# Performance work log

Measured on AMD Instinct MI355X. Metric: run time of the kernel, lower is better.

## Reference

```python
import jax, jax.numpy as jnp
import numpy as np

BN_EPS = 1e-5


def _get_normals(radius, nsample, xyz):
    # xyz: [B, N, 3] -> normals [B, N, 3] (eigenvector of smallest eigenvalue)
    B, N, _ = xyz.shape
    sq = jnp.sum(xyz * xyz, axis=-1)                      # [B, N]
    sqrdists = sq[:, :, None] + sq[:, None, :] - 2.0 * jnp.einsum('bnc,bmc->bnm', xyz, xyz)
    ar = jnp.arange(N, dtype=jnp.int32)
    group_idx = jnp.where(sqrdists > radius * radius, N, ar[None, None, :])  # [B, N, N]
    group_idx = jnp.sort(group_idx, axis=-1)[:, :, :nsample]                 # [B, N, ns]
    group_idx = jnp.where(group_idx == N, group_idx[:, :, :1], group_idx)
    group_points = jax.vmap(lambda pts, idx: pts[idx])(xyz, group_idx)       # [B, N, ns, 3]
    centered = group_points - group_points.mean(axis=2, keepdims=True)
    cov = jnp.einsum('bnsc,bnsd->bncd', centered, centered)                  # [B, N, 3, 3]
    _, eigen_vectors = jnp.linalg.eigh(cov)
    return eigen_vectors[..., 0]


def _conv_bn(h, w, b, g, be, m, v, relu=True):
    # h: [B, N, Cin]; 1x1 Conv1d == per-point linear; BN in eval mode
    h = h @ w.T + b
    h = (h - m) / jnp.sqrt(v + BN_EPS) * g + be
    return jax.nn.relu(h) if relu else h


def setup_inputs() -> dict:
    key = jax.random.key(0)
    ks = jax.random.split(key, 32)
    B, N = 4, 4096
    inp = {
        'x': jax.random.uniform(ks[0], (B, N, 3), dtype=jnp.float32),
        'small': 0.2,
        'large': 0.3,
    }
    chans = [(1, 16), (16, 32), (32, 16), (16, 1)]
    for li, (cin, cout) in enumerate(chans, start=1):
        k = 4 * li
        inp[f'w{li}'] = jax.random.normal(ks[k], (cout, cin), dtype=jnp.float32) * (1.0 / np.sqrt(cin))
        inp[f'b{li}'] = jax.random.normal(ks[k + 1], (cout,), dtype=jnp.float32) * 0.1
        inp[f'g{li}'] = jax.random.uniform(ks[k + 2], (cout,), dtype=jnp.float32) + 0.5
        inp[f'be{li}'] = jax.random.normal(ks[k + 3], (cout,), dtype=jnp.float32) * 0.1
        inp[f'm{li}'] = jnp.zeros((cout,), dtype=jnp.float32)
        inp[f'v{li}'] = jnp.ones((cout,), dtype=jnp.float32)
    return inp


def reference(x, small, large,
              w1, b1, g1, be1, m1, v1,
              w2, b2, g2, be2, m2, v2,
              w3, b3, g3, be3, m3, v3,
              w4, b4, g4, be4, m4, v4):
    xyz = x[:, :, :3]
    small_n = _get_normals(small, 32, xyz)   # [B, N, 3]
    large_n = _get_normals(large, 64, xyz)
    curvature = jnp.linalg.norm((small_n - large_n) * 0.5, axis=2)  # [B, N]
    h = curvature[..., None]                                        # [B, N, 1]
    h = _conv_bn(h, w1, b1, g1, be1, m1, v1)
    h = _conv_bn(h, w2, b2, g2, be2, m2, v2)
    h = _conv_bn(h, w3, b3, g3, be3, m3, v3)
    h = _conv_bn(h, w4, b4, g4, be4, m4, v4, relu=False)
    return h[..., 0]                                                # [B, N]
```

## Files before the change

### kernel.cpp

```cpp
#include <hip/hip_runtime.h>
#include <math.h>

#define BLAS_FMA 1
#define SYR2_VARIANT 0

#define DEV static __device__ __forceinline__

DEV float fA(float a, float b){ return __fadd_rn(a,b); }
DEV float fSb(float a, float b){ return __fsub_rn(a,b); }
DEV float fM(float a, float b){ return __fmul_rn(a,b); }
DEV float fDv(float a, float b){ return __fdiv_rn(a,b); }
DEV float fQ(float a){ return __fsqrt_rn(a); }
DEV float fF(float a, float b, float c){ return __builtin_fmaf(a,b,c); }
DEV float fSGN(float a, float b){ return copysignf(a,b); }

DEV float slapy2f(float x, float y){
  float xa=fabsf(x), ya=fabsf(y);
  float w=fmaxf(xa,ya), z=fminf(xa,ya);
  if (z==0.0f) return w;
  float t=fDv(z,w);
  return fM(w, fQ(fA(1.0f, fM(t,t))));
}

DEV void slartgf(float f, float g, float* c, float* s, float* r){
  const float safmin=1.17549435e-38f;
  const float safmax=8.50705917e+37f;
  const float rtmin=1.08420217e-19f;
  const float rtmax=6.52169543e+18f;
  float f1=fabsf(f), g1=fabsf(g);
  if (g==0.0f){ *c=1.0f; *s=0.0f; *r=f; }
  else if (f==0.0f){ *c=0.0f; *s=fSGN(1.0f,g); *r=g1; }
  else {
    if (f1>rtmin && f1<rtmax && g1>rtmin && g1<rtmax){
      float d=fQ(fA(fM(f,f), fM(g,g)));
      *c=fDv(f1,d);
      *r=fSGN(d,f);
      *s=fDv(g,*r);
    } else {
      float u=fminf(safmax, fmaxf(safmin, fmaxf(f1,g1)));
      float fs=fDv(f,u), gs=fDv(g,u);
      float d=fQ(fA(fM(fs,fs), fM(gs,gs)));
      *c=fDv(fabsf(fs), d);
      *r=fSGN(d,f);
      *s=fDv(gs,*r);
      *r=fM(*r,u);
    }
  }
}

DEV void slaev2f(float a, float b, float c, float* rt1, float* rt2, float* cs1, float* sn1){
  float sm=fA(a,c);
  float df=fSb(a,c);
  float adf=fabsf(df);
  float tb=fA(b,b);
  float ab=fabsf(tb);
  float acmx, acmn;
  if (fabsf(a)>fabsf(c)){ acmx=a; acmn=c; } else { acmx=c; acmn=a; }
  float rt;
  if (adf>ab){ float t=fDv(ab,adf); rt=fM(adf, fQ(fA(1.0f, fM(t,t)))); }
  else if (adf<ab){ float t=fDv(adf,ab); rt=fM(ab, fQ(fA(1.0f, fM(t,t)))); }
  else { rt=fM(ab, fQ(2.0f)); }
  int sgn1;
  if (sm<0.0f){
    *rt1=fM(0.5f, fSb(sm,rt)); sgn1=-1;
    *rt2=fSb(fM(fDv(acmx,*rt1),acmn), fM(fDv(b,*rt1),b));
  } else if (sm>0.0f){
    *rt1=fM(0.5f, fA(sm,rt)); sgn1=1;
    *rt2=fSb(fM(fDv(acmx,*rt1),acmn), fM(fDv(b,*rt1),b));
  } else {
    *rt1=fM(0.5f,rt); *rt2=fM(-0.5f,rt); sgn1=1;
  }
  float cs; int sgn2;
  if (df>=0.0f){ cs=fA(df,rt); sgn2=1; } else { cs=fSb(df,rt); sgn2=-1; }
  float acs=fabsf(cs);
  if (acs>ab){
    float ct=fDv(-tb,cs);
    *sn1=fDv(1.0f, fQ(fA(1.0f, fM(ct,ct))));
    *cs1=fM(ct,*sn1);
  } else {
    if (ab==0.0f){ *cs1=1.0f; *sn1=0.0f; }
    else {
      float tn=fDv(-cs,tb);
      *cs1=fDv(1.0f, fQ(fA(1.0f, fM(tn,tn))));
      *sn1=fM(tn,*cs1);
    }
  }
  if (sgn1==sgn2){ float tn=*cs1; *cs1=-(*sn1); *sn1=tn; }
}

DEV void eig3_smallest(float a00, float a10, float a20, float a11, float a21, float a22,
                       float* vout){
  const float RMIN=3.13916472e-16f;
  const float RMAX=3.18559313e+15f;
  float anrm=fmaxf(fabsf(a00), fmaxf(fabsf(a10), fmaxf(fabsf(a20),
             fmaxf(fabsf(a11), fmaxf(fabsf(a21), fabsf(a22))))));
  if (anrm>0.0f && anrm<RMIN){
    float sig=fDv(RMIN,anrm);
    a00=fM(a00,sig); a10=fM(a10,sig); a20=fM(a20,sig);
    a11=fM(a11,sig); a21=fM(a21,sig); a22=fM(a22,sig);
  } else if (anrm>RMAX){
    float sig=fDv(RMAX,anrm);
    a00=fM(a00,sig); a10=fM(a10,sig); a20=fM(a20,sig);
    a11=fM(a11,sig); a21=fM(a21,sig); a22=fM(a22,sig);
  }
  float d0,d1,d2, e0,e1;
  float tau1=0.0f, hv2=0.0f;
  {
    float xnorm=fabsf(a20);
    if (xnorm==0.0f){
      tau1=0.0f;
      d0=a00; d1=a11; d2=a22;
      e0=a10; e1=a21;
    } else {
      float alpha=a10;
      float beta=-fSGN(slapy2f(alpha,xnorm), alpha);
      tau1=fDv(fSb(beta,alpha), beta);
      float rs=fDv(1.0f, fSb(alpha,beta));
      hv2=fM(a20, rs);
      float t2a=fM(a21, hv2);
#if BLAS_FMA
      float w1=fF(tau1, t2a, fM(tau1, a11));
      float w2=fF(fM(tau1,hv2), a22, fM(tau1, a21));
      float sd=fF(hv2, w2, w1);
#else
      float w1=fA(fM(tau1,a11), fM(tau1,t2a));
      float w2=fA(fM(tau1,a21), fM(fM(tau1,hv2),a22));
      float sd=fA(w1, fM(w2,hv2));
#endif
      float al2=fM(fM(-0.5f,tau1), sd);
      float nw1=fA(w1, al2);
#if BLAS_FMA
      float nw2=fF(al2, hv2, w2);
#else
      float nw2=fA(w2, fM(al2,hv2));
#endif
      w1=nw1; w2=nw2;
      float b11, b21, b22;
#if SYR2_VARIANT==0
      b11=fA(a11, fM(-2.0f, w1));
      b21=fA(a21, fF(hv2, -w1, -w2));
      b22=fA(a22, fF(hv2, -w2, fM(w2, -hv2)));
#elif SYR2_VARIANT==1
      b11=fSb(fSb(a11, w1), w1);
      b21=fSb(fF(hv2, -w1, a21), w2);
      b22=fF(w2, -hv2, fF(hv2, -w2, a22));
#else
      b11=fA(fA(a11, -w1), -w1);
      b21=fA(fA(a21, fM(hv2,-w1)), -w2);
      b22=fA(fA(a22, fM(hv2,-w2)), fM(w2,-hv2));
#endif
      d0=a00; d1=b11; d2=b22;
      e0=beta; e1=b21;
    }
  }
  float z0=1.0f,z1=0.0f,z2=0.0f, z3=0.0f,z4=1.0f,z5=0.0f, z6=0.0f,z7=0.0f,z8=1.0f;

#define DGET(iA)   ((iA)==0?d0:((iA)==1?d1:d2))
#define DSET(iA,vA) do{ float _dsv=(vA); int _dsi=(iA); \
  d0=(_dsi==0)?_dsv:d0; d1=(_dsi==1)?_dsv:d1; d2=(_dsi==2)?_dsv:d2; }while(0)
#define EGET(iA)   ((iA)==0?e0:e1)
#define ESET(iA,vA) do{ float _esv=(vA); int _esi=(iA); \
  e0=(_esi==0)?_esv:e0; e1=(_esi==1)?_esv:e1; }while(0)
#define ZGET(rA,cA) ((cA)==0? ((rA)==0?z0:((rA)==1?z1:z2)) : ((cA)==1? ((rA)==0?z3:((rA)==1?z4:z5)) : ((rA)==0?z6:((rA)==1?z7:z8))))
#define ZSET(rA,cA,vA) do{ float _zsv=(vA); int _zsr=(rA), _zsc=(cA); \
  z0=(_zsr==0&&_zsc==0)?_zsv:z0; z1=(_zsr==1&&_zsc==0)?_zsv:z1; z2=(_zsr==2&&_zsc==0)?_zsv:z2; \
  z3=(_zsr==0&&_zsc==1)?_zsv:z3; z4=(_zsr==1&&_zsc==1)?_zsv:z4; z5=(_zsr==2&&_zsc==1)?_zsv:z5; \
  z6=(_zsr==0&&_zsc==2)?_zsv:z6; z7=(_zsr==1&&_zsc==2)?_zsv:z7; z8=(_zsr==2&&_zsc==2)?_zsv:z8; }while(0)
#define ZROT0(ccA,ssA) do{ float _zc=(ccA), _zs=(ssA); \
  float _t0=z3, _a0=z0; z3=fSb(fM(_zc,_t0),fM(_zs,_a0)); z0=fA(fM(_zs,_t0),fM(_zc,_a0)); \
  float _t1=z4, _a1=z1; z4=fSb(fM(_zc,_t1),fM(_zs,_a1)); z1=fA(fM(_zs,_t1),fM(_zc,_a1)); \
  float _t2=z5, _a2=z2; z5=fSb(fM(_zc,_t2),fM(_zs,_a2)); z2=fA(fM(_zs,_t2),fM(_zc,_a2)); }while(0)
#define ZROT1(ccA,ssA) do{ float _zc=(ccA), _zs=(ssA); \
  float _t0=z6, _a0=z3; z6=fSb(fM(_zc,_t0),fM(_zs,_a0)); z3=fA(fM(_zs,_t0),fM(_zc,_a0)); \
  float _t1=z7, _a1=z4; z7=fSb(fM(_zc,_t1),fM(_zs,_a1)); z4=fA(fM(_zs,_t1),fM(_zc,_a1)); \
  float _t2=z8, _a2=z5; z8=fSb(fM(_zc,_t2),fM(_zs,_a2)); z5=fA(fM(_zs,_t2),fM(_zc,_a2)); }while(0)
#define ZSWAPC(caA,cbA) do{ int _zwa=(caA), _zwb=(cbA); \
  _Pragma("unroll") \
  for (int _zwr=0;_zwr<3;++_zwr){ \
    float _zwta=ZGET(_zwr,_zwa); float _zwtb=ZGET(_zwr,_zwb); \
    ZSET(_zwr,_zwa,_zwtb); ZSET(_zwr,_zwb,_zwta); \
  } }while(0)

  const float EPS=5.96046448e-08f;
  const float EPS2=3.55271368e-15f;
  const float SAFMIN=1.17549435e-38f;
  const float SSFMAX=3.07445735e+18f;
  const float SSFMIN=3.05175781e-05f;
  int l1=1, jtot=0; const int nmaxit=90;
  bool skip_sort=false;
  while (l1<=3){
    if (l1>1) ESET(l1-2, 0.0f);
    int m=3;
    for (int mm=l1; mm<=2; ++mm){
      float tst=fabsf(EGET(mm-1));
      if (tst==0.0f){ m=mm; break; }
      if (tst<=fM(fM(fQ(fabsf(DGET(mm-1))), fQ(fabsf(DGET(mm)))), EPS)){ ESET(mm-1,0.0f); m=mm; break; }
    }
    int l=l1, lsv=l, lend=m, lendsv=m;
    l1=m+1;
    if (lend==l) continue;
    float anorm=fabsf(DGET(lend-1));
    for (int i=l; i<=lend-1; ++i){ anorm=fmaxf(anorm,fabsf(DGET(i-1))); anorm=fmaxf(anorm,fabsf(EGET(i-1))); }
    if (anorm==0.0f) continue;
    int iscale=0;
    if (anorm>SSFMAX){
      iscale=1; float mv=fDv(SSFMAX,anorm);
      for (int i=l;i<=lend;++i) DSET(i-1, fM(DGET(i-1),mv));
      for (int i=l;i<=lend-1;++i) ESET(i-1, fM(EGET(i-1),mv));
    } else if (anorm<SSFMIN){
      iscale=2; float mv=fDv(SSFMIN,anorm);
      for (int i=l;i<=lend;++i) DSET(i-1, fM(DGET(i-1),mv));
      for (int i=l;i<=lend-1;++i) ESET(i-1, fM(EGET(i-1),mv));
    }
    if (fabsf(DGET(lend-1))<fabsf(DGET(l-1))){ lend=lsv; l=lendsv; }
    if (lend>l){
      for (;;){
        int M=lend;
        if (l!=lend){
          for (int mm=l; mm<=lend-1; ++mm){
            float ee=fabsf(EGET(mm-1));
            float tst=fM(ee,ee);
            if (tst<=fA(fM(fM(EPS2,fabsf(DGET(mm-1))), fabsf(DGET(mm))), SAFMIN)){ M=mm; break; }
          }
        }
        if (M<lend) ESET(M-1,0.0f);
        float p=DGET(l-1);
        if (M==l){
          l+=1;
          if (l<=lend) continue; else break;
        }
        if (M==l+1){
          float rt1,rt2,cc,ss;
          if (l==1){
            slaev2f(d0, e0, d1, &rt1,&rt2,&cc,&ss);
            ZROT0(cc, ss);
            d0=rt1; d1=rt2; e0=0.0f;
          } else {
            slaev2f(d1, e1, d2, &rt1,&rt2,&cc,&ss);
            ZROT1(cc, ss);
            d1=rt1; d2=rt2; e1=0.0f;
          }
          l+=2;
          if (l<=lend) continue; else break;
        }
        if (jtot==nmaxit) break;
        ++jtot;
        float g=fDv(fSb(d1,p), fM(2.0f,e0));
        float r=slapy2f(g,1.0f);
        g=fA(fSb(d2,p), fDv(e0, fA(g, fSGN(r,g))));
        float s=1.0f, c=1.0f; p=0.0f;
        float cr0,cr1,sr0,sr1;
        {
          float f=fM(s,e1);
          float bb=fM(c,e1);
          slartgf(g,f,&c,&s,&r);
          g=fSb(d2,p);
          r=fA(fM(fSb(d1,g),s), fM(fM(2.0f,c),bb));
          p=fM(s,r);
          d2=fA(g,p);
          g=fSb(fM(c,r),bb);
          cr1=c; sr1=-s;
        }
        {
          float f=fM(s,e0);
          float bb=fM(c,e0);
          slartgf(g,f,&c,&s,&r);
          e1=r;
          g=fSb(d1,p);
          r=fA(fM(fSb(d0,g),s), fM(fM(2.0f,c),bb));
          p=fM(s,r);
          d1=fA(g,p);
          g=fSb(fM(c,r),bb);
          cr0=c; sr0=-s;
        }
        if (cr1!=1.0f || sr1!=0.0f) ZROT1(cr1, sr1);
        if (cr0!=1.0f || sr0!=0.0f) ZROT0(cr0, sr0);
        d0=fSb(d0,p);
        e0=g;
      }
    } else {
      for (;;){
        int M=lend;
        if (l!=lend){
          for (int mm=l; mm>=lend+1; --mm){
            float ee=fabsf(EGET(mm-2));
            float tst=fM(ee,ee);
            if (tst<=fA(fM(fM(EPS2,fabsf(DGET(mm-1))), fabsf(DGET(mm-2))), SAFMIN)){ M=mm; break; }
          }
        }
        if (M>lend) ESET(M-2,0.0f);
        float p=DGET(l-1);
        if (M==l){
          l-=1;
          if (l>=lend) continue; else break;
        }
        if (M==l-1){
          float rt1,rt2,cc,ss;
          if (l==3){
            slaev2f(d1, e1, d2, &rt1,&rt2,&cc,&ss);
            ZROT1(cc, ss);
            d1=rt1; d2=rt2; e1=0.0f;
          } else {
            slaev2f(d0, e0, d1, &rt1,&rt2,&cc,&ss);
            ZROT0(cc, ss);
            d0=rt1; d1=rt2; e0=0.0f;
          }
          l-=2;
          if (l>=lend) continue; else break;
        }
        if (jtot==nmaxit) break;
        ++jtot;
        float g=fDv(fSb(d1,p), fM(2.0f,e1));
        float r=slapy2f(g,1.0f);
        g=fA(fSb(d0,p), fDv(e1, fA(g, fSGN(r,g))));
        float s=1.0f, c=1.0f; p=0.0f;
        float cr0,cr1,sr0,sr1;
        {
          float f=fM(s,e0);
          float bb=fM(c,e0);
          slartgf(g,f,&c,&s,&r);
          g=fSb(d0,p);
          r=fA(fM(fSb(d1,g),s), fM(fM(2.0f,c),bb));
          p=fM(s,r);
          d0=fA(g,p);
          g=fSb(fM(c,r),bb);
          cr0=c; sr0=s;
        }
        {
          float f=fM(s,e1);
          float bb=fM(c,e1);
          slartgf(g,f,&c,&s,&r);
          e0=r;
          g=fSb(d1,p);
          r=fA(fM(fSb(d2,g),s), fM(fM(2.0f,c),bb));
          p=fM(s,r);
          d1=fA(g,p);
          g=fSb(fM(c,r),bb);
          cr1=c; sr1=s;
        }
        if (cr0!=1.0f || sr0!=0.0f) ZROT0(cr0, sr0);
        if (cr1!=1.0f || sr1!=0.0f) ZROT1(cr1, sr1);
        d2=fSb(d2,p);
        e1=g;
      }
    }
    if (iscale==1){
      float mv=fDv(anorm,SSFMAX);
      for (int i=lsv;i<=lendsv;++i) DSET(i-1, fM(DGET(i-1),mv));
      for (int i=lsv;i<=lendsv-1;++i) ESET(i-1, fM(EGET(i-1),mv));
    } else if (iscale==2){
      float mv=fDv(anorm,SSFMIN);
      for (int i=lsv;i<=lendsv;++i) DSET(i-1, fM(DGET(i-1),mv));
      for (int i=lsv;i<=lendsv-1;++i) ESET(i-1, fM(EGET(i-1),mv));
    }
    if (jtot>=nmaxit){ skip_sort=true; break; }
  }
  if (!skip_sort){
    for (int ii=2; ii<=3; ++ii){
      int i=ii-1, k=i; float p=DGET(i-1);
      for (int j=ii; j<=3; ++j) if (DGET(j-1)<p){ k=j; p=DGET(j-1); }
      if (k!=i){
        DSET(k-1, DGET(i-1)); DSET(i-1, p);
        ZSWAPC(i-1, k-1);
      }
    }
  }
  float o0=z0, o1=z1, o2=z2;
  if (tau1!=0.0f){
#if BLAS_FMA
    float wv=fF(hv2, o2, o1);
    float t2=fM(-tau1, wv);
    o1=fA(o1, t2);
    o2=fF(t2, hv2, o2);
#else
    float wv=fA(o1, fM(o2,hv2));
    float t2=fM(-tau1, wv);
    o1=fA(o1, t2);
    o2=fA(o2, fM(hv2,t2));
#endif
  }
  vout[0]=o0; vout[1]=o1; vout[2]=o2;
#undef DGET
#undef DSET
#undef EGET
#undef ESET
#undef ZGET
#undef ZSET
#undef ZROT0
#undef ZROT1
#undef ZSWAPC
}

struct KP {
  const float* x; const float* rs; const float* rl;
  const float *w1,*b1,*g1,*be1,*m1,*v1;
  const float *w2,*b2,*g2,*be2,*m2,*v2;
  const float *w3,*b3,*g3,*be3,*m3,*v3;
  const float *w4,*b4,*g4,*be4,*m4,*v4;
  float* out;
};

#define WS_STRIDE 128

__global__ __launch_bounds__(64) void scan_kernel(const float* __restrict__ x,
                                                  const float* __restrict__ rsp,
                                                  const float* __restrict__ rlp,
                                                  unsigned short* __restrict__ ws){
  const int lane=threadIdx.x;
  const int pt=blockIdx.x;
  const int b=pt>>12, n=pt&4095;
  const float* P=x+(size_t)b*(4096*3);
  const double rds=rint((double)rsp[0]*1e7)/1e7;
  const double rdl=rint((double)rlp[0]*1e7)/1e7;
  const float rr_s=(float)(rds*rds);
  const float rr_l=(float)(rdl*rdl);
  const float px=P[3*n], py=P[3*n+1], pz=P[3*n+2];
  const float sqn=fA(fA(fM(px,px),fM(py,py)),fM(pz,pz));
  unsigned short* w=ws+(size_t)pt*WS_STRIDE;
  int cs=0, cl=0;
  for (int c=0;c<64;++c){
    int j=c*64+lane;
    float qx=P[3*j], qy=P[3*j+1], qz=P[3*j+2];
    float sqj=fA(fA(fM(qx,qx),fM(qy,qy)),fM(qz,qz));
    float dot=fA(fA(fM(px,qx),fM(py,qy)),fM(pz,qz));
    float d2=fSb(fA(sqn,sqj), fM(2.0f,dot));
    bool pl=!(d2>rr_l);
    bool ps=!(d2>rr_s);
    unsigned long long bl=__ballot(pl);
    unsigned long long bs=__ballot(ps);
    unsigned long long ltm=(1ull<<lane)-1ull;
    int posl=cl+__popcll(bl&ltm);
    int poss=cs+__popcll(bs&ltm);
    if (pl&&posl<64) w[posl]=(unsigned short)j;
    if (ps&&poss<32) w[64+poss]=(unsigned short)j;
    cl+=__popcll(bl); if(cl>64) cl=64;
    cs+=__popcll(bs); if(cs>32) cs=32;
    if (cs>=32&&cl>=64) break;
  }
  if (lane==0){ w[96]=(unsigned short)cl; w[97]=(unsigned short)cs; }
}

__global__ __launch_bounds__(64) void momeig_kernel(KP kp,
                                                    const unsigned short* __restrict__ ws){
  const int lane=threadIdx.x;
  const int t=blockIdx.x*64+lane;
  const int p=t>>1, which=t&1;
  const int b=p>>12;
  const float* P=kp.x+(size_t)b*(4096*3);
  const unsigned char* recB=(const unsigned char*)(ws+(size_t)p*WS_STRIDE);
  const uint4* q=(const uint4*)(recB + (which? 0 : 128));
  uint4 v0=q[0], v1=q[1], v2=q[2], v3=q[3];
  uint4 v4=q[4], v5=q[5], v6=q[6], v7=q[7];
  const unsigned int cw=*(const unsigned int*)(recB+192);
  const int cnt = which? (int)(cw&0xFFFFu) : (int)(cw>>16);
  const int trip= which? 64 : 32;
  unsigned int a[32]={v0.x,v0.y,v0.z,v0.w, v1.x,v1.y,v1.z,v1.w,
                      v2.x,v2.y,v2.z,v2.w, v3.x,v3.y,v3.z,v3.w,
                      v4.x,v4.y,v4.z,v4.w, v5.x,v5.y,v5.z,v5.w,
                      v6.x,v6.y,v6.z,v6.w, v7.x,v7.y,v7.z,v7.w};
  const int j0=(int)(a[0]&0xFFFFu);

  float sx=0.0f, sy=0.0f, sz=0.0f;
#pragma unroll
  for (int k=0;k<64;++k){
    int raw=(k&1)? (int)(a[k>>1]>>16) : (int)(a[k>>1]&0xFFFFu);
    int idx=(k<cnt)? raw : j0;
    float cx=P[3*idx], cy=P[3*idx+1], cz=P[3*idx+2];
    float nx=fA(sx,cx), ny=fA(sy,cy), nz=fA(sz,cz);
    bool en=(k<trip);
    sx=en?nx:sx; sy=en?ny:sy; sz=en?nz:sz;
  }
  const float dv=which? 64.0f : 32.0f;
  const float mx=fDv(sx,dv), my=fDv(sy,dv), mz=fDv(sz,dv);

  float c0=0,c1=0,c2=0,c3=0,c4=0,c5=0;
#pragma unroll
  for (int k=0;k<64;++k){
    int raw=(k&1)? (int)(a[k>>1]>>16) : (int)(a[k>>1]&0xFFFFu);
    int idx=(k<cnt)? raw : j0;
    float cx=fSb(P[3*idx],mx), cy=fSb(P[3*idx+1],my), cz=fSb(P[3*idx+2],mz);
    float t0=fA(c0,fM(cx,cx)), t1=fA(c1,fM(cy,cx)), t2=fA(c2,fM(cz,cx));
    float t3=fA(c3,fM(cy,cy)), t4=fA(c4,fM(cz,cy)), t5=fA(c5,fM(cz,cz));
    bool en=(k<trip);
    c0=en?t0:c0; c1=en?t1:c1; c2=en?t2:c2;
    c3=en?t3:c3; c4=en?t4:c4; c5=en?t5:c5;
  }

  float v[3];
  eig3_smallest(c0,c1,c2,c3,c4,c5,v);

  float pn0=__shfl_xor(v[0],1);
  float pn1=__shfl_xor(v[1],1);
  float pn2=__shfl_xor(v[2],1);

  if ((lane&1)==0){
    float dx=fM(fSb(v[0],pn0),0.5f);
    float dy=fM(fSb(v[1],pn1),0.5f);
    float dz=fM(fSb(v[2],pn2),0.5f);
    float curv=fQ(fA(fA(fM(dx,dx),fM(dy,dy)),fM(dz,dz)));

    float h1[16];
#pragma unroll
    for (int j=0;j<16;++j){
      float a0=fA(fM(kp.w1[j],curv), kp.b1[j]);
      a0=fA(fM(fDv(fSb(a0,kp.m1[j]), fQ(fA(kp.v1[j],1e-5f))), kp.g1[j]), kp.be1[j]);
      h1[j]=fmaxf(a0,0.0f);
    }
    float h2[32];
#pragma unroll
    for (int j=0;j<32;++j){
      float a0=0.0f;
#pragma unroll
      for (int k=0;k<16;++k) a0=fF(h1[k], kp.w2[j*16+k], a0);
      a0=fA(a0, kp.b2[j]);
      a0=fA(fM(fDv(fSb(a0,kp.m2[j]), fQ(fA(kp.v2[j],1e-5f))), kp.g2[j]), kp.be2[j]);
      h2[j]=fmaxf(a0,0.0f);
    }
    float h3[16];
#pragma unroll
    for (int j=0;j<16;++j){
      float a0=0.0f;
#pragma unroll
      for (int k=0;k<32;++k) a0=fF(h2[k], kp.w3[j*32+k], a0);
      a0=fA(a0, kp.b3[j]);
      a0=fA(fM(fDv(fSb(a0,kp.m3[j]), fQ(fA(kp.v3[j],1e-5f))), kp.g3[j]), kp.be3[j]);
      h3[j]=fmaxf(a0,0.0f);
    }
    float o=0.0f;
#pragma unroll
    for (int k=0;k<16;++k) o=fF(h3[k], kp.w4[k], o);
    o=fA(o, kp.b4[0]);
    o=fA(fM(fDv(fSb(o,kp.m4[0]), fQ(fA(kp.v4[0],1e-5f))), kp.g4[0]), kp.be4[0]);
    kp.out[p]=o;
  }
}

__global__ __launch_bounds__(256) void freq_kernel(KP kp){
  __shared__ float sP[4096*3];
  __shared__ float sSq[4096];
  __shared__ unsigned short sIdxL[64][66];
  __shared__ unsigned short sIdxS[64][34];
  __shared__ unsigned char sCntL[64], sCntS[64];
  const int tid=threadIdx.x;
  const int lane=tid&63, wid=tid>>6;
  const int b=blockIdx.x>>6;
  const int n0=(blockIdx.x&63)*64;
  const float* P=kp.x+(size_t)b*(4096*3);
  for (int i=tid;i<4096*3;i+=256) sP[i]=P[i];
  for (int j=tid;j<4096;j+=256){
    float qx=P[3*j],qy=P[3*j+1],qz=P[3*j+2];
    sSq[j]=fA(fA(fM(qx,qx),fM(qy,qy)),fM(qz,qz));
  }
  __syncthreads();
  const double rds=rint((double)kp.rs[0]*1e7)/1e7;
  const double rdl=rint((double)kp.rl[0]*1e7)/1e7;
  const float rr_s=(float)(rds*rds);
  const float rr_l=(float)(rdl*rdl);
  for (int pi=0; pi<16; ++pi){
    const int pl_i=wid*16+pi;
    const int n=n0+pl_i;
    const float px=sP[3*n], py=sP[3*n+1], pz=sP[3*n+2];
    const float sqn=sSq[n];
    int cs=0, cl=0;
    for (int c=0;c<64;++c){
      int j=c*64+lane;
      float dot=fA(fA(fM(px,sP[3*j]),fM(py,sP[3*j+1])),fM(pz,sP[3*j+2]));
      float d2=fSb(fA(sqn,sSq[j]), fM(2.0f,dot));
      bool pl_=!(d2>rr_l);
      bool ps_=!(d2>rr_s);
      unsigned long long bl=__ballot(pl_);
      unsigned long long bs=__ballot(ps_);
      unsigned long long ltm=(1ull<<lane)-1ull;
      int posl=cl+__popcll(bl&ltm);
      int poss=cs+__popcll(bs&ltm);
      if (pl_&&posl<64) sIdxL[pl_i][posl]=(unsigned short)j;
      if (ps_&&poss<32) sIdxS[pl_i][poss]=(unsigned short)j;
      cl+=__popcll(bl); if(cl>64) cl=64;
      cs+=__popcll(bs); if(cs>32) cs=32;
      if (cs>=32&&cl>=64) break;
    }
    if (lane==0){ sCntL[pl_i]=(unsigned char)cl; sCntS[pl_i]=(unsigned char)cs; }
  }
  __syncthreads();
  if (lane<16){
    const int pl_i=wid*16+lane;
    const int ptg=blockIdx.x*64+pl_i;
    const int csn=sCntS[pl_i], cln=sCntL[pl_i];
    const int j0s=sIdxS[pl_i][0], j0l=sIdxL[pl_i][0];
    float ssx=0.0f,ssy=0.0f,ssz=0.0f, slx=0.0f,sly=0.0f,slz=0.0f;
    for (int k=0;k<32;++k){
      int idx=(k<csn)?(int)sIdxS[pl_i][k]:j0s;
      ssx=fA(ssx,sP[3*idx]); ssy=fA(ssy,sP[3*idx+1]); ssz=fA(ssz,sP[3*idx+2]);
    }
    for (int k=0;k<64;++k){
      int idx=(k<cln)?(int)sIdxL[pl_i][k]:j0l;
      slx=fA(slx,sP[3*idx]); sly=fA(sly,sP[3*idx+1]); slz=fA(slz,sP[3*idx+2]);
    }
    const float msx=fDv(ssx,32.0f), msy=fDv(ssy,32.0f), msz=fDv(ssz,32.0f);
    const float mlx=fDv(slx,64.0f), mly=fDv(sly,64.0f), mlz=fDv(slz,64.0f);
    float sc0=0,sc1=0,sc2=0,sc3=0,sc4=0,sc5=0;
    for (int k=0;k<32;++k){
      int idx=(k<csn)?(int)sIdxS[pl_i][k]:j0s;
      float cx=fSb(sP[3*idx],msx), cy=fSb(sP[3*idx+1],msy), cz=fSb(sP[3*idx+2],msz);
      sc0=fA(sc0,fM(cx,cx)); sc1=fA(sc1,fM(cy,cx)); sc2=fA(sc2,fM(cz,cx));
      sc3=fA(sc3,fM(cy,cy)); sc4=fA(sc4,fM(cz,cy)); sc5=fA(sc5,fM(cz,cz));
    }
    float lc0=0,lc1=0,lc2=0,lc3=0,lc4=0,lc5=0;
    for (int k=0;k<64;++k){
      int idx=(k<cln)?(int)sIdxL[pl_i][k]:j0l;
      float cx=fSb(sP[3*idx],mlx), cy=fSb(sP[3*idx+1],mly), cz=fSb(sP[3*idx+2],mlz);
      lc0=fA(lc0,fM(cx,cx)); lc1=fA(lc1,fM(cy,cx)); lc2=fA(lc2,fM(cz,cx));
      lc3=fA(lc3,fM(cy,cy)); lc4=fA(lc4,fM(cz,cy)); lc5=fA(lc5,fM(cz,cz));
    }
    float snv[3], lnv[3];
    eig3_smallest(sc0,sc1,sc2,sc3,sc4,sc5, snv);
    eig3_smallest(lc0,lc1,lc2,lc3,lc4,lc5, lnv);
    float dx=fM(fSb(snv[0],lnv[0]),0.5f);
    float dy=fM(fSb(snv[1],lnv[1]),0.5f);
    float dz=fM(fSb(snv[2],lnv[2]),0.5f);
    float curv=fQ(fA(fA(fM(dx,dx),fM(dy,dy)),fM(dz,dz)));
    float h1[16];
#pragma unroll
    for (int j=0;j<16;++j){
      float a0=fA(fM(kp.w1[j],curv), kp.b1[j]);
      a0=fA(fM(fDv(fSb(a0,kp.m1[j]), fQ(fA(kp.v1[j],1e-5f))), kp.g1[j]), kp.be1[j]);
      h1[j]=fmaxf(a0,0.0f);
    }
    float h2[32];
#pragma unroll
    for (int j=0;j<32;++j){
      float a0=0.0f;
#pragma unroll
      for (int k=0;k<16;++k) a0=fF(h1[k], kp.w2[j*16+k], a0);
      a0=fA(a0, kp.b2[j]);
      a0=fA(fM(fDv(fSb(a0,kp.m2[j]), fQ(fA(kp.v2[j],1e-5f))), kp.g2[j]), kp.be2[j]);
      h2[j]=fmaxf(a0,0.0f);
    }
    float h3[16];
#pragma unroll
    for (int j=0;j<16;++j){
      float a0=0.0f;
#pragma unroll
      for (int k=0;k<32;++k) a0=fF(h2[k], kp.w3[j*32+k], a0);
      a0=fA(a0, kp.b3[j]);
      a0=fA(fM(fDv(fSb(a0,kp.m3[j]), fQ(fA(kp.v3[j],1e-5f))), kp.g3[j]), kp.be3[j]);
      h3[j]=fmaxf(a0,0.0f);
    }
    float o=0.0f;
#pragma unroll
    for (int k=0;k<16;++k) o=fF(h3[k], kp.w4[k], o);
    o=fA(o, kp.b4[0]);
    o=fA(fM(fDv(fSb(o,kp.m4[0]), fQ(fA(kp.v4[0],1e-5f))), kp.g4[0]), kp.be4[0]);
    kp.out[ptg]=o;
  }
}

extern "C" void kernel_launch(void* const* d_in, const int* in_sizes, int n_in,
                              void* d_out, int out_size, void* d_ws, size_t ws_size,
                              hipStream_t stream){
  (void)n_in; (void)out_size;
  KP kp;
  kp.x  =(const float*)d_in[0];
  kp.rs =(const float*)d_in[1];
  kp.rl =(const float*)d_in[2];
  kp.w1 =(const float*)d_in[3];  kp.b1 =(const float*)d_in[4];  kp.g1 =(const float*)d_in[5];
  kp.be1=(const float*)d_in[6];  kp.m1 =(const float*)d_in[7];  kp.v1 =(const float*)d_in[8];
  kp.w2 =(const float*)d_in[9];  kp.b2 =(const float*)d_in[10]; kp.g2 =(const float*)d_in[11];
  kp.be2=(const float*)d_in[12]; kp.m2 =(const float*)d_in[13]; kp.v2 =(const float*)d_in[14];
  kp.w3 =(const float*)d_in[15]; kp.b3 =(const float*)d_in[16]; kp.g3 =(const float*)d_in[17];
  kp.be3=(const float*)d_in[18]; kp.m3 =(const float*)d_in[19]; kp.v3 =(const float*)d_in[20];
  kp.w4 =(const float*)d_in[21]; kp.b4 =(const float*)d_in[22]; kp.g4 =(const float*)d_in[23];
  kp.be4=(const float*)d_in[24]; kp.m4 =(const float*)d_in[25]; kp.v4 =(const float*)d_in[26];
  kp.out=(float*)d_out;
  const int BN=in_sizes[0]/3;
  const size_t ws_need=(size_t)BN*256;
  if (ws_size>=ws_need){
    unsigned short* wsA=(unsigned short*)d_ws;
    scan_kernel<<<BN, 64, 0, stream>>>(kp.x, kp.rs, kp.rl, wsA);
    momeig_kernel<<<BN/32, 64, 0, stream>>>(kp, wsA);
  } else {
    freq_kernel<<<BN/64, 256, 0, stream>>>(kp);
  }
}
```

Baseline: 179.2 us.

## Add SoA preprocessing pass and store neighbor coordinates instead of indices

Adds a pre-pass that turns the xyz points into structure-of-arrays form with precomputed squared norms, so the scan kernel reads points with coalesced loads and no longer recomputes the norms. The scan kernel now writes neighbor coordinates straight into a larger per-point record instead of 16-bit indices, so the moment/eigen kernel reads its neighbors contiguously rather than gathering them by index. In exchange the workspace grows about fourfold, there is one extra kernel launch, and the scan kernel issues more global writes.

```diff
diff --git a/kernel.cpp b/kernel.cpp
--- a/kernel.cpp
+++ b/kernel.cpp
@@ -400,28 +400,43 @@
   float* out;
 };
 
-#define WS_STRIDE 128
-
-__global__ __launch_bounds__(64) void scan_kernel(const float* __restrict__ x,
-                                                  const float* __restrict__ rsp,
+#define REC_F 296
+
+__global__ __launch_bounds__(256) void soa_kernel(const float* __restrict__ x,
+                                                  float* __restrict__ xs, float* __restrict__ ys,
+                                                  float* __restrict__ zs, float* __restrict__ sq,
+                                                  int BN){
+  int i=blockIdx.x*256+threadIdx.x;
+  if (i<BN){
+    float a=x[3*i], b=x[3*i+1], c=x[3*i+2];
+    xs[i]=a; ys[i]=b; zs[i]=c;
+    sq[i]=fA(fA(fM(a,a),fM(b,b)),fM(c,c));
+  }
+}
+
+__global__ __launch_bounds__(64) void scan_kernel(const float* __restrict__ rsp,
                                                   const float* __restrict__ rlp,
-                                                  unsigned short* __restrict__ ws){
+                                                  float* __restrict__ wsA,
+                                                  const float* __restrict__ xs,
+                                                  const float* __restrict__ ys,
+                                                  const float* __restrict__ zs,
+                                                  const float* __restrict__ sq){
   const int lane=threadIdx.x;
   const int pt=blockIdx.x;
   const int b=pt>>12, n=pt&4095;
-  const float* P=x+(size_t)b*(4096*3);
+  const int g0=b<<12;
   const double rds=rint((double)rsp[0]*1e7)/1e7;
   const double rdl=rint((double)rlp[0]*1e7)/1e7;
   const float rr_s=(float)(rds*rds);
   const float rr_l=(float)(rdl*rdl);
-  const float px=P[3*n], py=P[3*n+1], pz=P[3*n+2];
-  const float sqn=fA(fA(fM(px,px),fM(py,py)),fM(pz,pz));
-  unsigned short* w=ws+(size_t)pt*WS_STRIDE;
+  const float px=xs[g0+n], py=ys[g0+n], pz=zs[g0+n];
+  const float sqn=sq[g0+n];
+  float* w=wsA+(size_t)pt*REC_F;
   int cs=0, cl=0;
   for (int c=0;c<64;++c){
-    int j=c*64+lane;
-    float qx=P[3*j], qy=P[3*j+1], qz=P[3*j+2];
-    float sqj=fA(fA(fM(qx,qx),fM(qy,qy)),fM(qz,qz));
+    int gj=g0+c*64+lane;
+    float qx=xs[gj], qy=ys[gj], qz=zs[gj];
+    float sqj=sq[gj];
     float dot=fA(fA(fM(px,qx),fM(py,qy)),fM(pz,qz));
     float d2=fSb(fA(sqn,sqj), fM(2.0f,dot));
     bool pl=!(d2>rr_l);
@@ -431,41 +446,31 @@
     unsigned long long ltm=(1ull<<lane)-1ull;
     int posl=cl+__popcll(bl&ltm);
     int poss=cs+__popcll(bs&ltm);
-    if (pl&&posl<64) w[posl]=(unsigned short)j;
-    if (ps&&poss<32) w[64+poss]=(unsigned short)j;
+    if (pl&&posl<64){ w[posl*3]=qx; w[posl*3+1]=qy; w[posl*3+2]=qz; }
+    if (ps&&poss<32){ w[192+poss*3]=qx; w[192+poss*3+1]=qy; w[192+poss*3+2]=qz; }
     cl+=__popcll(bl); if(cl>64) cl=64;
     cs+=__popcll(bs); if(cs>32) cs=32;
     if (cs>=32&&cl>=64) break;
   }
-  if (lane==0){ w[96]=(unsigned short)cl; w[97]=(unsigned short)cs; }
+  if (lane==0){ ((unsigned*)w)[288]=(unsigned)cl | ((unsigned)cs<<16); }
 }
 
 __global__ __launch_bounds__(64) void momeig_kernel(KP kp,
-                                                    const unsigned short* __restrict__ ws){
+                                                    const float* __restrict__ wsA){
   const int lane=threadIdx.x;
   const int t=blockIdx.x*64+lane;
   const int p=t>>1, which=t&1;
-  const int b=p>>12;
-  const float* P=kp.x+(size_t)b*(4096*3);
-  const unsigned char* recB=(const unsigned char*)(ws+(size_t)p*WS_STRIDE);
-  const uint4* q=(const uint4*)(recB + (which? 0 : 128));
-  uint4 v0=q[0], v1=q[1], v2=q[2], v3=q[3];
-  uint4 v4=q[4], v5=q[5], v6=q[6], v7=q[7];
-  const unsigned int cw=*(const unsigned int*)(recB+192);
+  const float* rec=wsA+(size_t)p*REC_F;
+  const unsigned cw=((const unsigned*)rec)[288];
   const int cnt = which? (int)(cw&0xFFFFu) : (int)(cw>>16);
   const int trip= which? 64 : 32;
-  unsigned int a[32]={v0.x,v0.y,v0.z,v0.w, v1.x,v1.y,v1.z,v1.w,
-                      v2.x,v2.y,v2.z,v2.w, v3.x,v3.y,v3.z,v3.w,
-                      v4.x,v4.y,v4.z,v4.w, v5.x,v5.y,v5.z,v5.w,
-                      v6.x,v6.y,v6.z,v6.w, v7.x,v7.y,v7.z,v7.w};
-  const int j0=(int)(a[0]&0xFFFFu);
+  const float* cf = rec + (which? 0 : 192);
 
   float sx=0.0f, sy=0.0f, sz=0.0f;
 #pragma unroll
   for (int k=0;k<64;++k){
-    int raw=(k&1)? (int)(a[k>>1]>>16) : (int)(a[k>>1]&0xFFFFu);
-    int idx=(k<cnt)? raw : j0;
-    float cx=P[3*idx], cy=P[3*idx+1], cz=P[3*idx+2];
+    int kk=(k<cnt)? k : 0;
+    float cx=cf[3*kk], cy=cf[3*kk+1], cz=cf[3*kk+2];
     float nx=fA(sx,cx), ny=fA(sy,cy), nz=fA(sz,cz);
     bool en=(k<trip);
     sx=en?nx:sx; sy=en?ny:sy; sz=en?nz:sz;
@@ -476,9 +481,8 @@
   float c0=0,c1=0,c2=0,c3=0,c4=0,c5=0;
 #pragma unroll
   for (int k=0;k<64;++k){
-    int raw=(k&1)? (int)(a[k>>1]>>16) : (int)(a[k>>1]&0xFFFFu);
-    int idx=(k<cnt)? raw : j0;
-    float cx=fSb(P[3*idx],mx), cy=fSb(P[3*idx+1],my), cz=fSb(P[3*idx+2],mz);
+    int kk=(k<cnt)? k : 0;
+    float cx=fSb(cf[3*kk],mx), cy=fSb(cf[3*kk+1],my), cz=fSb(cf[3*kk+2],mz);
     float t0=fA(c0,fM(cx,cx)), t1=fA(c1,fM(cy,cx)), t2=fA(c2,fM(cz,cx));
     float t3=fA(c3,fM(cy,cy)), t4=fA(c4,fM(cz,cy)), t5=fA(c5,fM(cz,cz));
     bool en=(k<trip);
@@ -673,10 +677,16 @@
   kp.be4=(const float*)d_in[24]; kp.m4 =(const float*)d_in[25]; kp.v4 =(const float*)d_in[26];
   kp.out=(float*)d_out;
   const int BN=in_sizes[0]/3;
-  const size_t ws_need=(size_t)BN*256;
+  const size_t recBytes=(size_t)BN*(REC_F*4);
+  const size_t ws_need=recBytes+(size_t)BN*16;
   if (ws_size>=ws_need){
-    unsigned short* wsA=(unsigned short*)d_ws;
-    scan_kernel<<<BN, 64, 0, stream>>>(kp.x, kp.rs, kp.rl, wsA);
+    float* wsA=(float*)d_ws;
+    float* xs=(float*)((char*)d_ws+recBytes);
+    float* ys=xs+BN;
+    float* zs=ys+BN;
+    float* sqv=zs+BN;
+    soa_kernel<<<(BN+255)/256, 256, 0, stream>>>(kp.x, xs, ys, zs, sqv, BN);
+    scan_kernel<<<BN, 64, 0, stream>>>(kp.rs, kp.rl, wsA, xs, ys, zs, sqv);
     momeig_kernel<<<BN/32, 64, 0, stream>>>(kp, wsA);
   } else {
     freq_kernel<<<BN/64, 256, 0, stream>>>(kp);
```

Result: slower. 188.6 us (+5.2%).

## Precompute SoA coordinates and squared norms; spread momeig work over more blocks

Applied to the files above, without the earlier changes.

Adds a pre-pass kernel that converts the interleaved xyz points into separate x/y/z arrays plus a precomputed squared-norm array in the workspace. The scan kernel then reads coalesced per-component arrays instead of stride-3 loads and no longer recomputes each candidate's norm. The momeig kernel now uses only 16 active lanes per 64-thread block, with four times as many blocks, to spread the heavy eigen-solve work across more compute units. This costs an extra kernel launch, extra workspace, and 75% idle lanes in momeig.

```diff
diff --git a/kernel.cpp b/kernel.cpp
--- a/kernel.cpp
+++ b/kernel.cpp
@@ -402,26 +402,42 @@
 
 #define WS_STRIDE 128
 
-__global__ __launch_bounds__(64) void scan_kernel(const float* __restrict__ x,
-                                                  const float* __restrict__ rsp,
+__global__ __launch_bounds__(256) void soa_kernel(const float* __restrict__ x,
+                                                  float* __restrict__ xs, float* __restrict__ ys,
+                                                  float* __restrict__ zs, float* __restrict__ sq,
+                                                  int BN){
+  int i=blockIdx.x*256+threadIdx.x;
+  if (i<BN){
+    float a=x[3*i], b=x[3*i+1], c=x[3*i+2];
+    xs[i]=a; ys[i]=b; zs[i]=c;
+    sq[i]=fA(fA(fM(a,a),fM(b,b)),fM(c,c));
+  }
+}
+
+__global__ __launch_bounds__(64) void scan_kernel(const float* __restrict__ rsp,
                                                   const float* __restrict__ rlp,
-                                                  unsigned short* __restrict__ ws){
+                                                  unsigned short* __restrict__ ws,
+                                                  const float* __restrict__ xs,
+                                                  const float* __restrict__ ys,
+                                                  const float* __restrict__ zs,
+                                                  const float* __restrict__ sq){
   const int lane=threadIdx.x;
   const int pt=blockIdx.x;
   const int b=pt>>12, n=pt&4095;
-  const float* P=x+(size_t)b*(4096*3);
+  const int g0=b<<12;
   const double rds=rint((double)rsp[0]*1e7)/1e7;
   const double rdl=rint((double)rlp[0]*1e7)/1e7;
   const float rr_s=(float)(rds*rds);
   const float rr_l=(float)(rdl*rdl);
-  const float px=P[3*n], py=P[3*n+1], pz=P[3*n+2];
-  const float sqn=fA(fA(fM(px,px),fM(py,py)),fM(pz,pz));
+  const float px=xs[g0+n], py=ys[g0+n], pz=zs[g0+n];
+  const float sqn=sq[g0+n];
   unsigned short* w=ws+(size_t)pt*WS_STRIDE;
   int cs=0, cl=0;
   for (int c=0;c<64;++c){
     int j=c*64+lane;
-    float qx=P[3*j], qy=P[3*j+1], qz=P[3*j+2];
-    float sqj=fA(fA(fM(qx,qx),fM(qy,qy)),fM(qz,qz));
+    int gj=g0+j;
+    float qx=xs[gj], qy=ys[gj], qz=zs[gj];
+    float sqj=sq[gj];
     float dot=fA(fA(fM(px,qx),fM(py,qy)),fM(pz,qz));
     float d2=fSb(fA(sqn,sqj), fM(2.0f,dot));
     bool pl=!(d2>rr_l);
@@ -443,7 +459,8 @@
 __global__ __launch_bounds__(64) void momeig_kernel(KP kp,
                                                     const unsigned short* __restrict__ ws){
   const int lane=threadIdx.x;
-  const int t=blockIdx.x*64+lane;
+  if (lane>=16) return;
+  const int t=blockIdx.x*16+lane;
   const int p=t>>1, which=t&1;
   const int b=p>>12;
   const float* P=kp.x+(size_t)b*(4096*3);
@@ -673,11 +690,17 @@
   kp.be4=(const float*)d_in[24]; kp.m4 =(const float*)d_in[25]; kp.v4 =(const float*)d_in[26];
   kp.out=(float*)d_out;
   const int BN=in_sizes[0]/3;
-  const size_t ws_need=(size_t)BN*256;
+  const size_t recBytes=(size_t)BN*256;
+  const size_t ws_need=recBytes+(size_t)BN*16;
   if (ws_size>=ws_need){
     unsigned short* wsA=(unsigned short*)d_ws;
-    scan_kernel<<<BN, 64, 0, stream>>>(kp.x, kp.rs, kp.rl, wsA);
-    momeig_kernel<<<BN/32, 64, 0, stream>>>(kp, wsA);
+    float* xs=(float*)((char*)d_ws+recBytes);
+    float* ys=xs+BN;
+    float* zs=ys+BN;
+    float* sqv=zs+BN;
+    soa_kernel<<<(BN+255)/256, 256, 0, stream>>>(kp.x, xs, ys, zs, sqv, BN);
+    scan_kernel<<<BN, 64, 0, stream>>>(kp.rs, kp.rl, wsA, xs, ys, zs, sqv);
+    momeig_kernel<<<BN/8, 64, 0, stream>>>(kp, wsA);
   } else {
     freq_kernel<<<BN/64, 256, 0, stream>>>(kp);
   }
```

After: 193.3 us. 7.9% more time.
